# Performance work log

Hardware: AMD Instinct MI355X
Metric: run time of the kernel (lower is better)

Reference implementation:

```python
import jax, jax.numpy as jnp
import numpy as np

NUM_CLASSES = 2
THRESH = 0.5        # overlap_thresh
NEGPOS = 3          # neg:pos ratio
VAR = (0.1, 0.2)    # cfg['variance']
B, P, O = 64, 32768, 50


def point_form(p):
    # center-size [cx,cy,w,h] -> corner [xmin,ymin,xmax,ymax]
    return jnp.concatenate([p[:, :2] - p[:, 2:] * 0.5, p[:, :2] + p[:, 2:] * 0.5], axis=1)


def iou(a, b):
    # a [O,4], b [P,4] corner form -> [O,P]
    lt = jnp.maximum(a[:, None, :2], b[None, :, :2])
    rb = jnp.minimum(a[:, None, 2:], b[None, :, 2:])
    wh = jnp.clip(rb - lt, 0.0, None)
    inter = wh[..., 0] * wh[..., 1]
    area_a = ((a[:, 2] - a[:, 0]) * (a[:, 3] - a[:, 1]))[:, None]
    area_b = ((b[:, 2] - b[:, 0]) * (b[:, 3] - b[:, 1]))[None, :]
    return inter / (area_a + area_b - inter)


def encode(matched, priors_cs):
    g_cxcy = ((matched[:, :2] + matched[:, 2:]) * 0.5 - priors_cs[:, :2]) / (VAR[0] * priors_cs[:, 2:])
    g_wh = jnp.log((matched[:, 2:] - matched[:, :2]) / priors_cs[:, 2:]) / VAR[1]
    return jnp.concatenate([g_cxcy, g_wh], axis=1)


def match_one(truths, labels, priors_cs, priors_pt):
    ovl = iou(truths, priors_pt)                # [O,P]
    best_prior_idx = jnp.argmax(ovl, axis=1)    # [O] best prior per GT
    best_truth_ovl = jnp.max(ovl, axis=0)       # [P]
    best_truth_idx = jnp.argmax(ovl, axis=0)    # [P]
    best_truth_ovl = best_truth_ovl.at[best_prior_idx].set(2.0)
    best_truth_idx = best_truth_idx.at[best_prior_idx].set(jnp.arange(truths.shape[0]))
    matched = truths[best_truth_idx]            # [P,4]
    conf = jnp.where(best_truth_ovl < THRESH, 0, labels[best_truth_idx])
    return encode(matched, priors_cs), conf


def reference(arm_loc, arm_conf, odm_loc, odm_conf, priors, targets):
    loc_data, conf_data = arm_loc, arm_conf    # use_ARM=False -> ARM branch
    num, num_priors = loc_data.shape[0], loc_data.shape[1]
    truths = targets[..., :4]
    labels = (targets[..., 4] >= 0).astype(jnp.int32)   # num_classes == 2 binarization
    priors_pt = point_form(priors)
    loc_t, conf_t = jax.vmap(lambda t, l: match_one(t, l, priors, priors_pt))(truths, labels)
    loc_t = jax.lax.stop_gradient(loc_t)
    conf_t = jax.lax.stop_gradient(conf_t)
    pos = conf_t > 0                             # [B,P]
    # localization: smooth L1, summed over positives
    d = loc_data - loc_t
    ad = jnp.abs(d)
    sl1 = jnp.where(ad < 1.0, 0.5 * d * d, ad - 0.5)
    loss_l = jnp.sum(sl1 * pos[..., None].astype(loc_data.dtype))
    # per-prior conf loss for hard negative mining
    lse = jax.nn.logsumexp(conf_data, axis=-1)   # [B,P]
    picked = jnp.take_along_axis(conf_data, conf_t[..., None], axis=-1)[..., 0]
    lc = lse - picked                            # NLL per prior
    lc_mine = jnp.where(pos, 0.0, lc)            # zero positives before ranking
    order = jnp.argsort(-lc_mine, axis=1)        # descending sort
    rank = jnp.argsort(order, axis=1)            # rank of each prior
    num_pos = jnp.sum(pos, axis=1, keepdims=True)            # [B,1]
    num_neg = jnp.minimum(NEGPOS * num_pos, num_priors - 1)
    neg = rank < num_neg
    sel = (pos | neg).astype(conf_data.dtype)
    loss_c = jnp.sum(lc * sel)
    N = jnp.sum(num_pos).astype(loc_data.dtype)
    return loss_l / N, loss_c / N


def setup_inputs():
    key = jax.random.key(0)
    ks = jax.random.split(key, 8)
    arm_loc = jax.random.normal(ks[0], (B, P, 4), jnp.float32)
    arm_conf = jax.random.normal(ks[1], (B, P, NUM_CLASSES), jnp.float32)
    odm_loc = jax.random.normal(ks[2], (B, P, 4), jnp.float32)
    odm_conf = jax.random.normal(ks[3], (B, P, NUM_CLASSES), jnp.float32)
    # priors in center-size form
    p_cxcy = jax.random.uniform(ks[4], (P, 2), jnp.float32, 0.05, 0.95)
    p_wh = jax.random.uniform(ks[5], (P, 2), jnp.float32, 0.05, 0.5)
    priors = jnp.concatenate([p_cxcy, p_wh], axis=1)
    # GT boxes in corner form with valid extents, labels >= 0
    t_cxcy = jax.random.uniform(ks[6], (B, O, 2), jnp.float32, 0.2, 0.8)
    t_wh = jax.random.uniform(ks[7], (B, O, 2), jnp.float32, 0.05, 0.3)
    boxes = jnp.concatenate([t_cxcy - t_wh * 0.5, t_cxcy + t_wh * 0.5], axis=-1)
    targets = jnp.concatenate([boxes, jnp.ones((B, O, 1), jnp.float32)], axis=-1)
    return {"arm_loc": arm_loc, "arm_conf": arm_conf, "odm_loc": odm_loc,
            "odm_conf": odm_conf, "priors": priors, "targets": targets}
```

## Files before the change

### kernel.cpp

```cpp
#include <hip/hip_runtime.h>
#include <cstdint>

#pragma clang fp contract(off)

#define BB 64
#define PP 32768
#define OO 50
#define THRESH_F 0.5f
#define VAR0 0.1f
#define VAR1 0.2f
#define NEGPOS_I 3
#define SS 32
#define T1 4
#define NB0 2048
#define NB12 1024

typedef unsigned long long u64;

__global__ void k_zero(float4* __restrict__ dst, int n4) {
    int i = blockIdx.x * blockDim.x + threadIdx.x;
    if (i < n4) dst[i] = make_float4(0.f, 0.f, 0.f, 0.f);
}

#define DPP_MAX(x, ctrl, rmask)                                              \
    x = fmaxf(x, __int_as_float(__builtin_amdgcn_update_dpp(                 \
            0, __float_as_int(x), (ctrl), (rmask), 0xf, true)));

__global__ void __launch_bounds__(256, 8)
k_match(const float* __restrict__ priors, const float* __restrict__ targets,
        float* __restrict__ bto, int* __restrict__ bti, u64* __restrict__ bpm) {
    __shared__ float tr4[OO * 4];
    __shared__ float trA[OO];
    int b = blockIdx.y, tid = threadIdx.x;
    for (int i = tid; i < OO * 4; i += 256)
        tr4[i] = targets[(size_t)(b * OO + (i >> 2)) * 5 + (i & 3)];
    __syncthreads();
    if (tid < OO)
        trA[tid] = (tr4[tid*4+2] - tr4[tid*4]) * (tr4[tid*4+3] - tr4[tid*4+1]);
    __syncthreads();

    int p0 = blockIdx.x * (256 * T1) + tid * T1;
    float bx0[T1], by0[T1], bx1[T1], by1[T1], aB[T1];
#pragma unroll
    for (int j = 0; j < T1; ++j) {
        float4 pr = ((const float4*)priors)[p0 + j];
        bx0[j] = pr.x - pr.z * 0.5f; by0[j] = pr.y - pr.w * 0.5f;
        bx1[j] = pr.x + pr.z * 0.5f; by1[j] = pr.y + pr.w * 0.5f;
        aB[j] = (bx1[j] - bx0[j]) * (by1[j] - by0[j]);
    }
    float rbv[T1]; int rbi[T1];
#pragma unroll
    for (int j = 0; j < T1; ++j) { rbv[j] = -1.0f; rbi[j] = 0; }

    for (int t = 0; t < OO; ++t) {
        float t0 = tr4[t*4], t1v = tr4[t*4+1], t2 = tr4[t*4+2], t3 = tr4[t*4+3];
        float aA = trA[t];
        float cbv = -1.0f; int cbp = 0;
#pragma unroll
        for (int j = 0; j < T1; ++j) {
            float ltx = fmaxf(t0, bx0[j]), lty = fmaxf(t1v, by0[j]);
            float rbx = fminf(t2, bx1[j]), rby = fminf(t3, by1[j]);
            float wx = fmaxf(rbx - ltx, 0.f), wy = fmaxf(rby - lty, 0.f);
            float inter = wx * wy;
            float v = inter / (aA + aB[j] - inter);
            if (v > rbv[j]) { rbv[j] = v; rbi[j] = t; }
            if (v > cbv) { cbv = v; cbp = p0 + j; }
        }
        float x = cbv;
        DPP_MAX(x, 0x111, 0xf);
        DPP_MAX(x, 0x112, 0xf);
        DPP_MAX(x, 0x114, 0xf);
        DPP_MAX(x, 0x118, 0xf);
        DPP_MAX(x, 0x142, 0xa);
        DPP_MAX(x, 0x143, 0xc);
        float mv = __int_as_float(__builtin_amdgcn_readlane(__float_as_int(x), 63));
        unsigned long long msk = __ballot(cbv == mv);
        int lane = (int)__ffsll((long long)msk) - 1;
        int pwin = __builtin_amdgcn_readlane(cbp, lane);
        if ((tid & 63) == 0) {
            u64 pk = ((u64)__float_as_uint(mv) << 32) | (unsigned)(PP - pwin);
            atomicMax(&bpm[b * OO + t], pk);
        }
    }
    size_t bp = (size_t)b * PP + p0;
    ((float4*)bto)[bp >> 2] = make_float4(rbv[0], rbv[1], rbv[2], rbv[3]);
    ((int4*)bti)[bp >> 2]   = make_int4(rbi[0], rbi[1], rbi[2], rbi[3]);
}

__global__ void k_force(const u64* __restrict__ bpm,
                        float* __restrict__ bto, int* __restrict__ bti) {
    __shared__ int pidx[OO];
    int b = blockIdx.x, tid = threadIdx.x;
    if (tid < OO) pidx[tid] = PP - (int)(unsigned)(bpm[b * OO + tid] & 0xFFFFFFFFull);
    __syncthreads();
    if (tid == 0) {
        for (int j = 0; j < OO; ++j) {
            int p = pidx[j];
            bto[(size_t)b * PP + p] = 2.0f;
            bti[(size_t)b * PP + p] = j;
        }
    }
}

__global__ void __launch_bounds__(256)
k_loss(const float* __restrict__ arm_loc, const float* __restrict__ arm_conf,
       const float* __restrict__ priors, const float* __restrict__ targets,
       const float* __restrict__ bto, const int* __restrict__ bti,
       float* __restrict__ lcm, float* __restrict__ pll,
       float* __restrict__ pplc, int* __restrict__ pnp) {
    int b = blockIdx.y, s = blockIdx.x, tid = threadIdx.x;
    int p = s * 1024 + tid * 4;
    size_t bp = (size_t)b * PP + p;

    float4 ov4 = ((const float4*)bto)[bp >> 2];
    int4   ti4 = ((const int4*)bti)[bp >> 2];
    float4 ca  = ((const float4*)arm_conf)[bp >> 1];
    float4 cb  = ((const float4*)arm_conf)[(bp >> 1) + 1];
    float ovs[4] = {ov4.x, ov4.y, ov4.z, ov4.w};
    int   tis[4] = {ti4.x, ti4.y, ti4.z, ti4.w};
    float cs[8]  = {ca.x, ca.y, ca.z, ca.w, cb.x, cb.y, cb.z, cb.w};

    float ll = 0.0f, plc = 0.0f; int np = 0;
    float outv[4];
    for (int c = 0; c < 4; ++c) {
        int ti = tis[c];
        const float* tb = &targets[(size_t)(b * OO + ti) * 5];
        int label = (tb[4] >= 0.0f) ? 1 : 0;
        int conf = (ovs[c] < THRESH_F) ? 0 : label;
        float c0 = cs[c * 2], c1 = cs[c * 2 + 1];
        float m = fmaxf(c0, c1);
        float lse = logf(expf(c0 - m) + expf(c1 - m)) + m;
        float picked = (conf == 1) ? c1 : c0;
        float lc = lse - picked;
        bool pos = conf > 0;
        outv[c] = pos ? 0.0f : lc;
        if (pos) {
            np++; plc += lc;
            float4 pr = ((const float4*)priors)[p + c];
            float gx = ((tb[0] + tb[2]) * 0.5f - pr.x) / (VAR0 * pr.z);
            float gy = ((tb[1] + tb[3]) * 0.5f - pr.y) / (VAR0 * pr.w);
            float gw = logf((tb[2] - tb[0]) / pr.z) / VAR1;
            float gh = logf((tb[3] - tb[1]) / pr.w) / VAR1;
            float g[4] = {gx, gy, gw, gh};
            float4 ld = ((const float4*)arm_loc)[bp + c];
            float lds_[4] = {ld.x, ld.y, ld.z, ld.w};
            for (int q = 0; q < 4; ++q) {
                float d = lds_[q] - g[q];
                float ad = fabsf(d);
                ll += (ad < 1.0f) ? 0.5f * d * d : ad - 0.5f;
            }
        }
    }
    ((float4*)lcm)[bp >> 2] = make_float4(outv[0], outv[1], outv[2], outv[3]);

    __shared__ float s1[256], s2[256]; __shared__ int s3[256];
    s1[tid] = ll; s2[tid] = plc; s3[tid] = np;
    __syncthreads();
    for (int st = 128; st > 0; st >>= 1) {
        if (tid < st) { s1[tid] += s1[tid+st]; s2[tid] += s2[tid+st]; s3[tid] += s3[tid+st]; }
        __syncthreads();
    }
    if (tid == 0) {
        pll[s * BB + b] = s1[0];
        pplc[s * BB + b] = s2[0];
        pnp[s * BB + b] = s3[0];
    }
}

template <int PASS>
__global__ void __launch_bounds__(256)
k_hist(const float* __restrict__ lcm, const unsigned* __restrict__ spre,
       int* __restrict__ Hc, float* __restrict__ Hs) {
    const int nbins = (PASS == 0) ? NB0 : NB12;
    __shared__ int hc[NB0]; __shared__ float hs[NB0];
    int b = blockIdx.y, tid = threadIdx.x;
    for (int i = tid; i < nbins; i += 256) { hc[i] = 0; hs[i] = 0.f; }
    __syncthreads();
    unsigned pref = (PASS == 0) ? 0u : spre[b];
    const float4* v4 = (const float4*)(lcm + (size_t)b * PP);
    int base = blockIdx.x * 1024;
    for (int i = 0; i < 4; ++i) {
        float4 x = v4[base + i * 256 + tid];
        float xs[4] = {x.x, x.y, x.z, x.w};
        for (int c = 0; c < 4; ++c) {
            unsigned u = __float_as_uint(xs[c]);
            bool ok; unsigned bin;
            if (PASS == 0)      { ok = true;               bin = u >> 20; }
            else if (PASS == 1) { ok = (u >> 20) == pref;  bin = (u >> 10) & 1023u; }
            else                { ok = (u >> 10) == pref;  bin = u & 1023u; }
            if (ok) { atomicAdd(&hc[bin], 1); atomicAdd(&hs[bin], xs[c]); }
        }
    }
    __syncthreads();
    for (int i = tid; i < nbins; i += 256) {
        int cv = hc[i];
        if (cv) {
            atomicAdd(&Hc[b * nbins + i], cv);
            atomicAdd(&Hs[b * nbins + i], hs[i]);
        }
    }
}

__global__ void __launch_bounds__(256)
k_scan(const int* __restrict__ Hc, const float* __restrict__ Hs, int nbins,
       int pass, const int* __restrict__ pnp, unsigned* __restrict__ spre,
       int* __restrict__ srem, float* __restrict__ ssum,
       unsigned* __restrict__ stb) {
    int b = blockIdx.x, tid = threadIdx.x;
    int CH = nbins >> 8;
    const int* hc = Hc + b * nbins;
    const float* hs = Hs + b * nbins;
    __shared__ int sc[256]; __shared__ float sf[256];
    __shared__ int s_chunk; __shared__ int s_r; __shared__ float s_S;

    int c = 0; float f = 0.f;
    int base = tid * CH;
    for (int i = 0; i < CH; ++i) { c += hc[base + i]; f += hs[base + i]; }
    sc[tid] = c; sf[tid] = f;
    __syncthreads();
    for (int off = 1; off < 256; off <<= 1) {
        int cv = (tid + off < 256) ? sc[tid + off] : 0;
        float fv = (tid + off < 256) ? sf[tid + off] : 0.f;
        __syncthreads();
        sc[tid] += cv; sf[tid] += fv;
        __syncthreads();
    }
    if (tid == 0) {
        int r; float S;
        if (pass == 0) {
            int np = 0;
            for (int i = 0; i < SS; ++i) np += pnp[i * BB + b];
            int k = NEGPOS_I * np; if (k > PP - 1) k = PP - 1;
            r = k; S = 0.f;
        } else { r = srem[b]; S = ssum[b]; }
        s_r = r; s_S = S;
    }
    __syncthreads();
    int r = s_r;
    int nxt = (tid == 255) ? 0 : sc[tid + 1];
    if (sc[tid] >= r && nxt < r) s_chunk = tid;
    __syncthreads();
    if (tid == 0) {
        int ch = s_chunk;
        int r2 = r - ((ch == 255) ? 0 : sc[ch + 1]);
        float S2 = s_S + ((ch == 255) ? 0.f : sf[ch + 1]);
        int binSel = ch * CH;
        for (int i = CH - 1; i >= 0; --i) {
            int bin = ch * CH + i;
            int cb = hc[bin];
            if (r2 <= cb) { binSel = bin; break; }
            r2 -= cb; S2 += hs[bin];
        }
        unsigned pref = (pass == 0) ? (unsigned)binSel
                                    : ((spre[b] << 10) | (unsigned)binSel);
        spre[b] = pref; srem[b] = r2; ssum[b] = S2;
        if (pass == 2) stb[b] = pref;
    }
}

__global__ void k_final(const float* __restrict__ pll, const float* __restrict__ pplc,
                        const int* __restrict__ pnp, const float* __restrict__ ssum,
                        const int* __restrict__ srem, const unsigned* __restrict__ stb,
                        float* __restrict__ out) {
    int b = threadIdx.x;
    float ll = 0.f, plc = 0.f; int np = 0;
    for (int s = 0; s < SS; ++s) {
        ll += pll[s * BB + b];
        plc += pplc[s * BB + b];
        np += pnp[s * BB + b];
    }
    float tval = __uint_as_float(stb[b]);
    float cc = plc + ssum[b] + (float)srem[b] * tval;
    for (int s = 32; s > 0; s >>= 1) {
        ll += __shfl_down(ll, s);
        cc += __shfl_down(cc, s);
        np += __shfl_down(np, s);
    }
    if (b == 0) {
        float N = (float)np;
        out[0] = ll / N;
        out[1] = cc / N;
    }
}

extern "C" void kernel_launch(void* const* d_in, const int* in_sizes, int n_in,
                              void* d_out, int out_size, void* d_ws, size_t ws_size,
                              hipStream_t stream) {
    const float* arm_loc  = (const float*)d_in[0];
    const float* arm_conf = (const float*)d_in[1];
    const float* priors   = (const float*)d_in[4];
    const float* targets  = (const float*)d_in[5];
    float* out = (float*)d_out;

    char* w = (char*)d_ws;
    float* bto = (float*)w;  w += sizeof(float) * (size_t)BB * PP;
    int*   bti = (int*)w;    w += sizeof(int)   * (size_t)BB * PP;
    float* lcm = (float*)w;  w += sizeof(float) * (size_t)BB * PP;
    char* zbase = w;
    int*   Hc0 = (int*)w;    w += sizeof(int)   * BB * NB0;
    float* Hs0 = (float*)w;  w += sizeof(float) * BB * NB0;
    int*   Hc1 = (int*)w;    w += sizeof(int)   * BB * NB12;
    float* Hs1 = (float*)w;  w += sizeof(float) * BB * NB12;
    int*   Hc2 = (int*)w;    w += sizeof(int)   * BB * NB12;
    float* Hs2 = (float*)w;  w += sizeof(float) * BB * NB12;
    u64*   bpm = (u64*)w;    w += sizeof(u64)   * BB * OO;
    size_t zbytes = (size_t)(w - zbase);
    float* pll  = (float*)w; w += sizeof(float) * BB * SS;
    float* pplc = (float*)w; w += sizeof(float) * BB * SS;
    int*   pnp  = (int*)w;   w += sizeof(int)   * BB * SS;
    unsigned* spre = (unsigned*)w; w += sizeof(unsigned) * BB;
    int*      srem = (int*)w;      w += sizeof(int) * BB;
    float*    ssum = (float*)w;    w += sizeof(float) * BB;
    unsigned* stb  = (unsigned*)w; w += sizeof(unsigned) * BB;

    int n4 = (int)(zbytes / 16);
    k_zero<<<(n4 + 255) / 256, 256, 0, stream>>>((float4*)zbase, n4);
    k_match<<<dim3(PP / (256 * T1), BB), 256, 0, stream>>>(priors, targets, bto, bti, bpm);
    k_force<<<BB, 64, 0, stream>>>(bpm, bto, bti);
    k_loss<<<dim3(SS, BB), 256, 0, stream>>>(arm_loc, arm_conf, priors, targets,
                                             bto, bti, lcm, pll, pplc, pnp);
    k_hist<0><<<dim3(8, BB), 256, 0, stream>>>(lcm, spre, Hc0, Hs0);
    k_scan<<<BB, 256, 0, stream>>>(Hc0, Hs0, NB0, 0, pnp, spre, srem, ssum, stb);
    k_hist<1><<<dim3(8, BB), 256, 0, stream>>>(lcm, spre, Hc1, Hs1);
    k_scan<<<BB, 256, 0, stream>>>(Hc1, Hs1, NB12, 1, pnp, spre, srem, ssum, stb);
    k_hist<2><<<dim3(8, BB), 256, 0, stream>>>(lcm, spre, Hc2, Hs2);
    k_scan<<<BB, 256, 0, stream>>>(Hc2, Hs2, NB12, 2, pnp, spre, srem, ssum, stb);
    k_final<<<1, 64, 0, stream>>>(pll, pplc, pnp, ssum, srem, stb, out);
}
```

Baseline: 283.4 us.

## Fuse first histogram pass into loss kernel and precompute target boxes

```diff
diff --git a/kernel.cpp b/kernel.cpp
--- a/kernel.cpp
+++ b/kernel.cpp
@@ -17,27 +17,39 @@
 
 typedef unsigned long long u64;
 
-__global__ void k_zero(float4* __restrict__ dst, int n4) {
-    int i = blockIdx.x * blockDim.x + threadIdx.x;
-    if (i < n4) dst[i] = make_float4(0.f, 0.f, 0.f, 0.f);
+__global__ void k_zero(float4* __restrict__ dst, int n4,
+                       const float* __restrict__ targets,
+                       float4* __restrict__ trT, float* __restrict__ trAr) {
+    if (blockIdx.y == 0) {
+        int i = blockIdx.x * blockDim.x + threadIdx.x;
+        if (i < n4) dst[i] = make_float4(0.f, 0.f, 0.f, 0.f);
+    } else {
+        int b = blockIdx.x, t = threadIdx.x;
+        if (b < BB && t < OO) {
+            const float* tb = &targets[(size_t)(b * OO + t) * 5];
+            float x0 = tb[0], y0 = tb[1], x1 = tb[2], y1 = tb[3];
+            trT[b * OO + t] = make_float4(x0, y0, x1, y1);
+            trAr[b * OO + t] = (x1 - x0) * (y1 - y0);
+        }
+        if (b == 0 && t == 0) {
+            trT[BB * OO] = make_float4(0.f, 0.f, 0.f, 0.f);
+            trAr[BB * OO] = 1.0f;
+        }
+    }
 }
 
 #define DPP_MAX(x, ctrl, rmask)                                              \
-    x = fmaxf(x, __int_as_float(__builtin_amdgcn_update_dpp(                 \
-            0, __float_as_int(x), (ctrl), (rmask), 0xf, true)));
+    {                                                                        \
+        int _o = __float_as_int(x);                                          \
+        x = fmaxf(x, __int_as_float(__builtin_amdgcn_update_dpp(             \
+                _o, _o, (ctrl), (rmask), 0xf, false)));                      \
+    }
 
 __global__ void __launch_bounds__(256, 8)
-k_match(const float* __restrict__ priors, const float* __restrict__ targets,
+k_match(const float* __restrict__ priors, const float4* __restrict__ trT,
+        const float* __restrict__ trAr,
         float* __restrict__ bto, int* __restrict__ bti, u64* __restrict__ bpm) {
-    __shared__ float tr4[OO * 4];
-    __shared__ float trA[OO];
     int b = blockIdx.y, tid = threadIdx.x;
-    for (int i = tid; i < OO * 4; i += 256)
-        tr4[i] = targets[(size_t)(b * OO + (i >> 2)) * 5 + (i & 3)];
-    __syncthreads();
-    if (tid < OO)
-        trA[tid] = (tr4[tid*4+2] - tr4[tid*4]) * (tr4[tid*4+3] - tr4[tid*4+1]);
-    __syncthreads();
 
     int p0 = blockIdx.x * (256 * T1) + tid * T1;
     float bx0[T1], by0[T1], bx1[T1], by1[T1], aB[T1];
@@ -52,9 +64,15 @@
 #pragma unroll
     for (int j = 0; j < T1; ++j) { rbv[j] = -1.0f; rbi[j] = 0; }
 
+    int tb0 = b * OO;
+    float4 tt = trT[tb0];
+    float aA = trAr[tb0];
+
     for (int t = 0; t < OO; ++t) {
-        float t0 = tr4[t*4], t1v = tr4[t*4+1], t2 = tr4[t*4+2], t3 = tr4[t*4+3];
-        float aA = trA[t];
+        float4 ttn = trT[tb0 + t + 1];
+        float aAn = trAr[tb0 + t + 1];
+
+        float t0 = tt.x, t1v = tt.y, t2 = tt.z, t3 = tt.w;
         float cbv = -1.0f; int cbp = 0;
 #pragma unroll
         for (int j = 0; j < T1; ++j) {
@@ -81,6 +99,7 @@
             u64 pk = ((u64)__float_as_uint(mv) << 32) | (unsigned)(PP - pwin);
             atomicMax(&bpm[b * OO + t], pk);
         }
+        tt = ttn; aA = aAn;
     }
     size_t bp = (size_t)b * PP + p0;
     ((float4*)bto)[bp >> 2] = make_float4(rbv[0], rbv[1], rbv[2], rbv[3]);
@@ -89,16 +108,17 @@
 
 __global__ void k_force(const u64* __restrict__ bpm,
                         float* __restrict__ bto, int* __restrict__ bti) {
-    __shared__ int pidx[OO];
-    int b = blockIdx.x, tid = threadIdx.x;
-    if (tid < OO) pidx[tid] = PP - (int)(unsigned)(bpm[b * OO + tid] & 0xFFFFFFFFull);
-    __syncthreads();
-    if (tid == 0) {
-        for (int j = 0; j < OO; ++j) {
-            int p = pidx[j];
-            bto[(size_t)b * PP + p] = 2.0f;
-            bti[(size_t)b * PP + p] = j;
-        }
+    int b = blockIdx.x, j = threadIdx.x;
+    int p = -1;
+    if (j < OO) p = PP - (int)(unsigned)(bpm[b * OO + j] & 0xFFFFFFFFull);
+    bool w = (j < OO);
+    for (int jj = 1; jj < OO; ++jj) {
+        int pj = __shfl(p, jj, 64);
+        if (jj > j && pj == p) w = false;
+    }
+    if (w) {
+        bto[(size_t)b * PP + p] = 2.0f;
+        bti[(size_t)b * PP + p] = j;
     }
 }
 
@@ -107,8 +127,13 @@
        const float* __restrict__ priors, const float* __restrict__ targets,
        const float* __restrict__ bto, const int* __restrict__ bti,
        float* __restrict__ lcm, float* __restrict__ pll,
-       float* __restrict__ pplc, int* __restrict__ pnp) {
+       float* __restrict__ pplc, int* __restrict__ pnp,
+       int* __restrict__ Hc0, float* __restrict__ Hs0) {
+    __shared__ int hc[NB0]; __shared__ float hs[NB0];
     int b = blockIdx.y, s = blockIdx.x, tid = threadIdx.x;
+    for (int i = tid; i < NB0; i += 256) { hc[i] = 0; hs[i] = 0.f; }
+    __syncthreads();
+
     int p = s * 1024 + tid * 4;
     size_t bp = (size_t)b * PP + p;
 
@@ -150,6 +175,9 @@
                 ll += (ad < 1.0f) ? 0.5f * d * d : ad - 0.5f;
             }
         }
+        unsigned u = __float_as_uint(outv[c]);
+        atomicAdd(&hc[u >> 20], 1);
+        atomicAdd(&hs[u >> 20], outv[c]);
     }
     ((float4*)lcm)[bp >> 2] = make_float4(outv[0], outv[1], outv[2], outv[3]);
 
@@ -165,38 +193,39 @@
         pplc[s * BB + b] = s2[0];
         pnp[s * BB + b] = s3[0];
     }
+    for (int i = tid; i < NB0; i += 256) {
+        int cv = hc[i];
+        if (cv) {
+            atomicAdd(&Hc0[b * NB0 + i], cv);
+            atomicAdd(&Hs0[b * NB0 + i], hs[i]);
+        }
+    }
 }
 
 template <int PASS>
 __global__ void __launch_bounds__(256)
 k_hist(const float* __restrict__ lcm, const unsigned* __restrict__ spre,
        int* __restrict__ Hc, float* __restrict__ Hs) {
-    const int nbins = (PASS == 0) ? NB0 : NB12;
-    __shared__ int hc[NB0]; __shared__ float hs[NB0];
+    __shared__ int hc[NB12]; __shared__ float hs[NB12];
     int b = blockIdx.y, tid = threadIdx.x;
-    for (int i = tid; i < nbins; i += 256) { hc[i] = 0; hs[i] = 0.f; }
-    __syncthreads();
-    unsigned pref = (PASS == 0) ? 0u : spre[b];
-    const float4* v4 = (const float4*)(lcm + (size_t)b * PP);
-    int base = blockIdx.x * 1024;
-    for (int i = 0; i < 4; ++i) {
-        float4 x = v4[base + i * 256 + tid];
-        float xs[4] = {x.x, x.y, x.z, x.w};
-        for (int c = 0; c < 4; ++c) {
-            unsigned u = __float_as_uint(xs[c]);
-            bool ok; unsigned bin;
-            if (PASS == 0)      { ok = true;               bin = u >> 20; }
-            else if (PASS == 1) { ok = (u >> 20) == pref;  bin = (u >> 10) & 1023u; }
-            else                { ok = (u >> 10) == pref;  bin = u & 1023u; }
-            if (ok) { atomicAdd(&hc[bin], 1); atomicAdd(&hs[bin], xs[c]); }
-        }
-    }
-    __syncthreads();
-    for (int i = tid; i < nbins; i += 256) {
+    for (int i = tid; i < NB12; i += 256) { hc[i] = 0; hs[i] = 0.f; }
+    __syncthreads();
+    unsigned pref = spre[b];
+    float4 x = ((const float4*)(lcm + (size_t)b * PP))[blockIdx.x * 256 + tid];
+    float xs[4] = {x.x, x.y, x.z, x.w};
+    for (int c = 0; c < 4; ++c) {
+        unsigned u = __float_as_uint(xs[c]);
+        bool ok; unsigned bin;
+        if (PASS == 1) { ok = (u >> 20) == pref;  bin = (u >> 10) & 1023u; }
+        else           { ok = (u >> 10) == pref;  bin = u & 1023u; }
+        if (ok) { atomicAdd(&hc[bin], 1); atomicAdd(&hs[bin], xs[c]); }
+    }
+    __syncthreads();
+    for (int i = tid; i < NB12; i += 256) {
         int cv = hc[i];
         if (cv) {
-            atomicAdd(&Hc[b * nbins + i], cv);
-            atomicAdd(&Hs[b * nbins + i], hs[i]);
+            atomicAdd(&Hc[b * NB12 + i], cv);
+            atomicAdd(&Hs[b * NB12 + i], hs[i]);
         }
     }
 }
@@ -312,18 +341,20 @@
     int*      srem = (int*)w;      w += sizeof(int) * BB;
     float*    ssum = (float*)w;    w += sizeof(float) * BB;
     unsigned* stb  = (unsigned*)w; w += sizeof(unsigned) * BB;
+    float4* trT = (float4*)w;      w += sizeof(float4) * (BB * OO + 1);
+    float*  trAr = (float*)w;      w += sizeof(float)  * (BB * OO + 1);
 
     int n4 = (int)(zbytes / 16);
-    k_zero<<<(n4 + 255) / 256, 256, 0, stream>>>((float4*)zbase, n4);
-    k_match<<<dim3(PP / (256 * T1), BB), 256, 0, stream>>>(priors, targets, bto, bti, bpm);
+    int nzb = (n4 + 255) / 256; if (nzb < BB) nzb = BB;
+    k_zero<<<dim3(nzb, 2), 256, 0, stream>>>((float4*)zbase, n4, targets, trT, trAr);
+    k_match<<<dim3(PP / (256 * T1), BB), 256, 0, stream>>>(priors, trT, trAr, bto, bti, bpm);
     k_force<<<BB, 64, 0, stream>>>(bpm, bto, bti);
     k_loss<<<dim3(SS, BB), 256, 0, stream>>>(arm_loc, arm_conf, priors, targets,
-                                             bto, bti, lcm, pll, pplc, pnp);
-    k_hist<0><<<dim3(8, BB), 256, 0, stream>>>(lcm, spre, Hc0, Hs0);
+                                             bto, bti, lcm, pll, pplc, pnp, Hc0, Hs0);
     k_scan<<<BB, 256, 0, stream>>>(Hc0, Hs0, NB0, 0, pnp, spre, srem, ssum, stb);
-    k_hist<1><<<dim3(8, BB), 256, 0, stream>>>(lcm, spre, Hc1, Hs1);
+    k_hist<1><<<dim3(32, BB), 256, 0, stream>>>(lcm, spre, Hc1, Hs1);
     k_scan<<<BB, 256, 0, stream>>>(Hc1, Hs1, NB12, 1, pnp, spre, srem, ssum, stb);
-    k_hist<2><<<dim3(8, BB), 256, 0, stream>>>(lcm, spre, Hc2, Hs2);
+    k_hist<2><<<dim3(32, BB), 256, 0, stream>>>(lcm, spre, Hc2, Hs2);
     k_scan<<<BB, 256, 0, stream>>>(Hc2, Hs2, NB12, 2, pnp, spre, srem, ssum, stb);
     k_final<<<1, 64, 0, stream>>>(pll, pplc, pnp, ssum, srem, stb, out);
 }
```

Measured after the change: 275.8 us. -2.7%, faster.
